# Kernel tuning notes

Measured on AMD Instinct MI355X. Metric: run time of the kernel, lower is better.

The kernel has to match this reference:

```python
import jax, jax.numpy as jnp
import numpy as np

T, OBS, H, NOBJ = 32768, 256, 512, 4


def _xavier(key, shape):
    fan_in, fan_out = shape[0], shape[1]
    lim = jnp.sqrt(6.0 / (fan_in + fan_out)).astype(jnp.float32)
    return jax.random.uniform(key, shape, jnp.float32, -lim, lim)


def setup_inputs() -> dict:
    key = jax.random.key(0)
    ks = jax.random.split(key, 16)
    # weights stored as [in, out] so y = x @ W (same math as nn.Linear with W.T)
    return {
        "x": jax.random.normal(ks[0], (T, OBS), jnp.float32),
        "W_in0": _xavier(ks[1], (OBS, H)),
        "W_B0": _xavier(ks[2], (OBS, H)),
        "W_C0": _xavier(ks[3], (OBS, H)),
        "W_d0": _xavier(ks[4], (OBS, H)),
        "A_log0": jax.random.normal(ks[5], (H,), jnp.float32),
        "W_in1": _xavier(ks[6], (H, H)),
        "W_B1": _xavier(ks[7], (H, H)),
        "W_C1": _xavier(ks[8], (H, H)),
        "W_d1": _xavier(ks[9], (H, H)),
        "A_log1": jax.random.normal(ks[10], (H,), jnp.float32),
        "W_out": _xavier(ks[11], (H, NOBJ)),
        "b_out": jnp.zeros((NOBJ,), jnp.float32),
        "W_skip": _xavier(ks[12], (OBS, NOBJ)),
    }


def _mamba_layer(x, W_in, W_B, W_C, W_d, A_log):
    # x: [T, D_in] -> [T, H]
    x_state = x @ W_in           # [T, H]
    B = x @ W_B                  # [T, H]
    C = x @ W_C                  # [T, H]
    delta = jax.nn.sigmoid(x @ W_d)  # [T, H]
    A = -jnp.exp(A_log)          # [H]
    A_bar = jnp.exp(delta * A)   # [T, H], in (0, 1)
    Bx = B * x_state             # [T, H]

    def step(h, inp):
        a_t, bx_t = inp
        h = a_t * h + bx_t
        return h, h

    h0 = jnp.zeros((x_state.shape[-1],), x_state.dtype)
    _, h_seq = jax.lax.scan(step, h0, (A_bar, Bx))  # [T, H]
    return C * h_seq


def reference(x, W_in0, W_B0, W_C0, W_d0, A_log0,
              W_in1, W_B1, W_C1, W_d1, A_log1,
              W_out, b_out, W_skip):
    skip = x
    y = _mamba_layer(x, W_in0, W_B0, W_C0, W_d0, A_log0)
    y = _mamba_layer(y, W_in1, W_B1, W_C1, W_d1, A_log1)
    out = y @ W_out + b_out + skip @ W_skip  # [T, NOBJ]
    return out
```

## Files before the change

### kernel.cpp

```cpp
#include <hip/hip_runtime.h>

typedef __attribute__((ext_vector_type(8))) short short8;
typedef __attribute__((ext_vector_type(4))) float floatx4;

#define T_SIZE 32768
#define OBS    256
#define H      512
#define NC     1024
#define CHUNK  32
#define NGRP   64
#define GCH    16

__device__ __forceinline__ unsigned short f2bf(float f){
    union { float f; unsigned u; } v; v.f = f;
    unsigned u = v.u;
    u += 0x7FFFu + ((u >> 16) & 1u);
    return (unsigned short)(u >> 16);
}
__device__ __forceinline__ float bf2f(unsigned short u){
    union { unsigned u; float f; } v; v.u = ((unsigned)u) << 16; return v.f;
}

#define GLOAD_LDS16(g, l) \
    __builtin_amdgcn_global_load_lds((const __attribute__((address_space(1))) unsigned*)(g), \
                                     (__attribute__((address_space(3))) unsigned*)(l), 16, 0, 0)

__global__ void prep_kernel(const float* __restrict__ x, unsigned short* __restrict__ xb,
                            const float* __restrict__ A0W0, const float* __restrict__ A0W1,
                            const float* __restrict__ A0W2, const float* __restrict__ A0W3,
                            unsigned short* __restrict__ Wt0,
                            const float* __restrict__ A1W0, const float* __restrict__ A1W1,
                            const float* __restrict__ A1W2, const float* __restrict__ A1W3,
                            unsigned short* __restrict__ Wt1){
    const int b = blockIdx.x;
    const int tid = threadIdx.x;
    if (b < 8192){
        int i = b * 256 + tid;
        float4 v = ((const float4*)x)[i];
        ushort4 o;
        o.x = f2bf(v.x); o.y = f2bf(v.y); o.z = f2bf(v.z); o.w = f2bf(v.w);
        ((ushort4*)xb)[i] = o;
    } else if (b < 10240){
        const int K = OBS, KH = OBS * H;
        int idx = (b - 8192) * 256 + tid;
        int s   = idx / KH;
        int rem = idx - s * KH;
        int h = rem >> 8;
        int k = rem & 255;
        const float* W = (s == 0) ? A0W0 : (s == 1) ? A0W1 : (s == 2) ? A0W2 : A0W3;
        int bb = h >> 4, hh = h & 15;
        Wt0[(size_t)((bb * 4 + s) * 16 + hh) * K + k] = f2bf(W[(size_t)k * H + h]);
    } else {
        const int K = H, KH = H * H;
        int idx = (b - 10240) * 256 + tid;
        int s   = idx / KH;
        int rem = idx - s * KH;
        int h = rem >> 9;
        int k = rem & 511;
        const float* W = (s == 0) ? A1W0 : (s == 1) ? A1W1 : (s == 2) ? A1W2 : A1W3;
        int bb = h >> 4, hh = h & 15;
        Wt1[(size_t)((bb * 4 + s) * 16 + hh) * K + k] = f2bf(W[(size_t)k * H + h]);
    }
}

template<int K>
__global__ __launch_bounds__(256, 3) void gemm_layer_kernel(
    const unsigned short* __restrict__ xb,
    const unsigned short* __restrict__ wt,
    const float* __restrict__ A_log,
    unsigned short* __restrict__ gT, unsigned short* __restrict__ bxT, unsigned short* __restrict__ CT,
    float* __restrict__ Pbuf, float* __restrict__ Hbuf,
    float* __restrict__ Pm, float* __restrict__ Hm)
{
    __shared__ unsigned short SM[3][8192];

    const int tid  = threadIdx.x;
    const int wave = tid >> 6;
    const int lane = tid & 63;
    const int ml   = lane & 15;
    const int quad = lane >> 4;
    const int wm   = wave & 1;
    const int wn   = wave >> 1;

    const int flat = blockIdx.y * 16 + blockIdx.x;
    const int xcd  = flat & 7;
    const int j    = flat >> 3;
    const int nb   = j & 15;
    const int mb   = (j >> 4) * 8 + xcd;
    const int m0   = mb * 128;

    const int srow = tid >> 2;
    const int sel  = (((tid & 3) ^ ((tid >> 3) & 3))) * 8;
    const int swz  = (ml >> 1) & 3;

    const unsigned short* pa0 = xb + (size_t)(m0 + srow) * K + sel;
    const unsigned short* pa1 = pa0 + (size_t)64 * K;
    const unsigned short* pb0 = wt + (size_t)(nb * 128 + srow) * K + sel;
    const unsigned short* pb1 = pb0 + (size_t)64 * K;

    const int ldsA0 = (wave * 64 + 0  ) * 8;
    const int ldsA1 = (wave * 64 + 256) * 8;

    const int rbaseA = (wm * 64 + ml) * 32 + (quad ^ swz) * 8;
    const int rbaseB = (wn * 64 + ml) * 32 + (quad ^ swz) * 8;

    floatx4 acc[4][4];
    #pragma unroll
    for (int i = 0; i < 4; i++)
        #pragma unroll
        for (int jj = 0; jj < 4; jj++)
            acc[i][jj] = (floatx4)(0.0f);

    constexpr int NK = K >> 5;

#define STAGE(kt_) { const int b_ = (kt_) % 3; const int ko_ = (kt_) * 32; \
        GLOAD_LDS16(pa0 + ko_, &SM[b_][ldsA0]); \
        GLOAD_LDS16(pa1 + ko_, &SM[b_][ldsA1]); \
        GLOAD_LDS16(pb0 + ko_, &SM[b_][4096 + ldsA0]); \
        GLOAD_LDS16(pb1 + ko_, &SM[b_][4096 + ldsA1]); }

    STAGE(0); STAGE(1);
    asm volatile("s_waitcnt vmcnt(4)" ::: "memory");
    __builtin_amdgcn_s_barrier();
    __builtin_amdgcn_sched_barrier(0);

    #pragma unroll
    for (int kk = 0; kk < NK; ++kk){
        const int cur = kk % 3;

        if (kk + 2 < NK) STAGE(kk + 2);

        short8 av[4], bv[4];
        #pragma unroll
        for (int i = 0; i < 4; i++)
            av[i] = *(const short8*)(&SM[cur][0] + rbaseA + i * 16 * 32);
        #pragma unroll
        for (int jj = 0; jj < 4; jj++)
            bv[jj] = *(const short8*)(&SM[cur][4096] + rbaseB + jj * 16 * 32);

        __builtin_amdgcn_s_setprio(1);
        #pragma unroll
        for (int i = 0; i < 4; i++)
            #pragma unroll
            for (int jj = 0; jj < 4; jj++)
                acc[i][jj] = __builtin_amdgcn_mfma_f32_16x16x32_bf16(av[i], bv[jj], acc[i][jj], 0, 0, 0);
        __builtin_amdgcn_s_setprio(0);

        if (kk + 1 < NK){
            if (kk + 2 < NK) { asm volatile("s_waitcnt vmcnt(4)" ::: "memory"); }
            else             { asm volatile("s_waitcnt vmcnt(0)" ::: "memory"); }
            __builtin_amdgcn_s_barrier();
            __builtin_amdgcn_sched_barrier(0);
        }
    }
    __syncthreads();

#undef STAGE

    unsigned short* SMe = &SM[0][0];
    float2* segbuf = (float2*)(SMe + 12288);
    const int col = wn * 16 + ml;
    const int h   = nb * 32 + col;
    const float Aneg = -expf(A_log[h]);

    #pragma unroll
    for (int i = 0; i < 4; i++){
        float p = 1.0f, hh = 0.0f;
        #pragma unroll
        for (int r = 0; r < 4; r++){
            int trow = wm * 64 + i * 16 + quad * 4 + r;
            float dv = acc[i][3][r];
            float delta = 1.0f / (1.0f + expf(-dv));
            unsigned short gb = f2bf(delta * Aneg);
            float a = __expf(bf2f(gb));
            unsigned short bb = f2bf(acc[i][1][r] * acc[i][0][r]);
            SMe[        trow * 32 + col] = gb;
            SMe[4096 +  trow * 32 + col] = bb;
            SMe[8192 +  trow * 32 + col] = f2bf(acc[i][2][r]);
            hh = fmaf(a, hh, bf2f(bb));
            p *= a;
        }
        const int ch = wm * 2 + (i >> 1);
        const int s  = (i & 1) * 4 + quad;
        segbuf[(ch * 8 + s) * 32 + col] = make_float2(p, hh);
    }
    __syncthreads();
    {
        const short8* s8 = (const short8*)SMe;
        #pragma unroll
        for (int arr = 0; arr < 3; arr++){
            unsigned short* bp = (arr == 0) ? gT : (arr == 1) ? bxT : CT;
            #pragma unroll
            for (int half = 0; half < 2; half++){
                int u = half * 256 + tid;
                int row = u >> 2, part = u & 3;
                *(short8*)(bp + (size_t)(m0 + row) * H + nb * 32 + part * 8) = s8[arr * 512 + u];
            }
        }
    }
    if (tid < 128){
        const int ccol = tid & 31, ch = tid >> 5;
        const int c = mb * 4 + ch;
        float P = 1.0f, Hc = 0.0f;
        #pragma unroll
        for (int s = 0; s < 4; s++){
            float2 ph = segbuf[(ch * 8 + s) * 32 + ccol];
            Hc = fmaf(ph.x, Hc, ph.y);
            P *= ph.x;
        }
        Pm[(size_t)c * H + nb * 32 + ccol] = P;
        Hm[(size_t)c * H + nb * 32 + ccol] = Hc;
        #pragma unroll
        for (int s = 4; s < 8; s++){
            float2 ph = segbuf[(ch * 8 + s) * 32 + ccol];
            Hc = fmaf(ph.x, Hc, ph.y);
            P *= ph.x;
        }
        Pbuf[(size_t)c * H + nb * 32 + ccol] = P;
        Hbuf[(size_t)c * H + nb * 32 + ccol] = Hc;
    }
}

__global__ void scan2a_kernel(const float* __restrict__ P, const float* __restrict__ Hc,
                              float* __restrict__ Pg, float* __restrict__ Hg){
    const int g  = blockIdx.x;
    const int j4 = threadIdx.x * 4;
    float4 pc = {1.f,1.f,1.f,1.f}, hc = {0.f,0.f,0.f,0.f};
    #pragma unroll
    for (int i = 0; i < GCH; i++){
        size_t o = (size_t)(g * GCH + i) * H + j4;
        float4 P4 = *(const float4*)(P + o);
        float4 H4 = *(const float4*)(Hc + o);
        hc.x = fmaf(P4.x, hc.x, H4.x); pc.x *= P4.x;
        hc.y = fmaf(P4.y, hc.y, H4.y); pc.y *= P4.y;
        hc.z = fmaf(P4.z, hc.z, H4.z); pc.z *= P4.z;
        hc.w = fmaf(P4.w, hc.w, H4.w); pc.w *= P4.w;
    }
    *(float4*)(Pg + (size_t)g * H + j4) = pc;
    *(float4*)(Hg + (size_t)g * H + j4) = hc;
}

__global__ __launch_bounds__(256) void scan3_kernel(
    const unsigned short* __restrict__ gT, const unsigned short* __restrict__ bxT,
    const unsigned short* __restrict__ CT,
    const float* __restrict__ P, const float* __restrict__ Hc,
    const float* __restrict__ Pm, const float* __restrict__ Hm,
    const float* __restrict__ Pg, const float* __restrict__ Hg,
    unsigned short* __restrict__ yb){
    const int c    = blockIdx.x;
    const int half = threadIdx.x >> 7;
    const int j4   = (threadIdx.x & 127) * 4;
    const int grp  = c >> 4;
    float4 h = {0.f, 0.f, 0.f, 0.f};
    for (int g = 0; g < grp; ++g){
        float4 P4 = *(const float4*)(Pg + (size_t)g * H + j4);
        float4 H4 = *(const float4*)(Hg + (size_t)g * H + j4);
        h.x = fmaf(P4.x, h.x, H4.x);
        h.y = fmaf(P4.y, h.y, H4.y);
        h.z = fmaf(P4.z, h.z, H4.z);
        h.w = fmaf(P4.w, h.w, H4.w);
    }
    for (int cc = grp << 4; cc < c; ++cc){
        float4 P4 = *(const float4*)(P + (size_t)cc * H + j4);
        float4 H4 = *(const float4*)(Hc + (size_t)cc * H + j4);
        h.x = fmaf(P4.x, h.x, H4.x);
        h.y = fmaf(P4.y, h.y, H4.y);
        h.z = fmaf(P4.z, h.z, H4.z);
        h.w = fmaf(P4.w, h.w, H4.w);
    }
    if (half){
        float4 P4 = *(const float4*)(Pm + (size_t)c * H + j4);
        float4 H4 = *(const float4*)(Hm + (size_t)c * H + j4);
        h.x = fmaf(P4.x, h.x, H4.x);
        h.y = fmaf(P4.y, h.y, H4.y);
        h.z = fmaf(P4.z, h.z, H4.z);
        h.w = fmaf(P4.w, h.w, H4.w);
    }
    size_t off = (size_t)(c * CHUNK + half * 16) * H + j4;
    #pragma unroll 8
    for (int i = 0; i < 16; i++){
        ushort4 gv = *(const ushort4*)(gT + off);
        ushort4 bv = *(const ushort4*)(bxT + off);
        ushort4 cv = *(const ushort4*)(CT + off);
        h.x = fmaf(__expf(bf2f(gv.x)), h.x, bf2f(bv.x));
        h.y = fmaf(__expf(bf2f(gv.y)), h.y, bf2f(bv.y));
        h.z = fmaf(__expf(bf2f(gv.z)), h.z, bf2f(bv.z));
        h.w = fmaf(__expf(bf2f(gv.w)), h.w, bf2f(bv.w));
        ushort4 o;
        o.x = f2bf(bf2f(cv.x) * h.x);
        o.y = f2bf(bf2f(cv.y) * h.y);
        o.z = f2bf(bf2f(cv.z) * h.z);
        o.w = f2bf(bf2f(cv.w) * h.w);
        *(ushort4*)(yb + off) = o;
        off += H;
    }
}

__global__ __launch_bounds__(256) void scan3f_kernel(
    const unsigned short* __restrict__ gT, const unsigned short* __restrict__ bxT,
    const unsigned short* __restrict__ CT,
    const float* __restrict__ P, const float* __restrict__ Hc,
    const float* __restrict__ Pm, const float* __restrict__ Hm,
    const float* __restrict__ Pg, const float* __restrict__ Hg,
    const unsigned short* __restrict__ xb,
    const float* __restrict__ Wout, const float* __restrict__ bout,
    const float* __restrict__ Wskip,
    float* __restrict__ out){
    __shared__ unsigned short ystage[32 * 512];
    const int tid  = threadIdx.x;
    const int c    = blockIdx.x;
    const int half = tid >> 7;
    const int j4   = (tid & 127) * 4;
    const int grp  = c >> 4;
    float4 h = {0.f, 0.f, 0.f, 0.f};
    for (int g = 0; g < grp; ++g){
        float4 P4 = *(const float4*)(Pg + (size_t)g * H + j4);
        float4 H4 = *(const float4*)(Hg + (size_t)g * H + j4);
        h.x = fmaf(P4.x, h.x, H4.x);
        h.y = fmaf(P4.y, h.y, H4.y);
        h.z = fmaf(P4.z, h.z, H4.z);
        h.w = fmaf(P4.w, h.w, H4.w);
    }
    for (int cc = grp << 4; cc < c; ++cc){
        float4 P4 = *(const float4*)(P + (size_t)cc * H + j4);
        float4 H4 = *(const float4*)(Hc + (size_t)cc * H + j4);
        h.x = fmaf(P4.x, h.x, H4.x);
        h.y = fmaf(P4.y, h.y, H4.y);
        h.z = fmaf(P4.z, h.z, H4.z);
        h.w = fmaf(P4.w, h.w, H4.w);
    }
    if (half){
        float4 P4 = *(const float4*)(Pm + (size_t)c * H + j4);
        float4 H4 = *(const float4*)(Hm + (size_t)c * H + j4);
        h.x = fmaf(P4.x, h.x, H4.x);
        h.y = fmaf(P4.y, h.y, H4.y);
        h.z = fmaf(P4.z, h.z, H4.z);
        h.w = fmaf(P4.w, h.w, H4.w);
    }
    size_t off = (size_t)(c * CHUNK + half * 16) * H + j4;
    #pragma unroll 8
    for (int i = 0; i < 16; i++){
        ushort4 gv = *(const ushort4*)(gT + off);
        ushort4 bv = *(const ushort4*)(bxT + off);
        ushort4 cv = *(const ushort4*)(CT + off);
        h.x = fmaf(__expf(bf2f(gv.x)), h.x, bf2f(bv.x));
        h.y = fmaf(__expf(bf2f(gv.y)), h.y, bf2f(bv.y));
        h.z = fmaf(__expf(bf2f(gv.z)), h.z, bf2f(bv.z));
        h.w = fmaf(__expf(bf2f(gv.w)), h.w, bf2f(bv.w));
        ushort4 o;
        o.x = f2bf(bf2f(cv.x) * h.x);
        o.y = f2bf(bf2f(cv.y) * h.y);
        o.z = f2bf(bf2f(cv.z) * h.z);
        o.w = f2bf(bf2f(cv.w) * h.w);
        *(ushort4*)(&ystage[(half * 16 + i) * 512 + j4]) = o;
        off += H;
    }
    __syncthreads();

    const int wave = tid >> 6;
    const int lane = tid & 63;
    const float4* W4 = (const float4*)Wout;
    const float4* S4 = (const float4*)Wskip;
    const float b0 = bout[0], b1 = bout[1], b2 = bout[2], b3 = bout[3];
    for (int rr = 0; rr < 8; ++rr){
        const int r = wave * 8 + rr;
        const int t = c * 32 + r;
        float s0 = 0.f, s1 = 0.f, s2 = 0.f, s3 = 0.f;
        #pragma unroll
        for (int k = lane; k < H; k += 64){
            float yv = bf2f(ystage[r * 512 + k]);
            float4 w = W4[k];
            s0 = fmaf(yv, w.x, s0); s1 = fmaf(yv, w.y, s1);
            s2 = fmaf(yv, w.z, s2); s3 = fmaf(yv, w.w, s3);
        }
        #pragma unroll
        for (int k = lane; k < OBS; k += 64){
            float xv = bf2f(xb[(size_t)t * OBS + k]);
            float4 w = S4[k];
            s0 = fmaf(xv, w.x, s0); s1 = fmaf(xv, w.y, s1);
            s2 = fmaf(xv, w.z, s2); s3 = fmaf(xv, w.w, s3);
        }
        #pragma unroll
        for (int o = 32; o > 0; o >>= 1){
            s0 += __shfl_down(s0, o);
            s1 += __shfl_down(s1, o);
            s2 += __shfl_down(s2, o);
            s3 += __shfl_down(s3, o);
        }
        if (lane == 0){
            out[(size_t)t * 4 + 0] = s0 + b0;
            out[(size_t)t * 4 + 1] = s1 + b1;
            out[(size_t)t * 4 + 2] = s2 + b2;
            out[(size_t)t * 4 + 3] = s3 + b3;
        }
    }
}

extern "C" void kernel_launch(void* const* d_in, const int* in_sizes, int n_in,
                              void* d_out, int out_size, void* d_ws, size_t ws_size,
                              hipStream_t stream)
{
    const float* x     = (const float*)d_in[0];
    const float* W_in0 = (const float*)d_in[1];
    const float* W_B0  = (const float*)d_in[2];
    const float* W_C0  = (const float*)d_in[3];
    const float* W_d0  = (const float*)d_in[4];
    const float* A0    = (const float*)d_in[5];
    const float* W_in1 = (const float*)d_in[6];
    const float* W_B1  = (const float*)d_in[7];
    const float* W_C1  = (const float*)d_in[8];
    const float* W_d1  = (const float*)d_in[9];
    const float* A1    = (const float*)d_in[10];
    const float* Wout  = (const float*)d_in[11];
    const float* bout  = (const float*)d_in[12];
    const float* Wskip = (const float*)d_in[13];
    float* out = (float*)d_out;

    char* ws = (char*)d_ws;
    size_t off = 0;
    auto alloc = [&](size_t bytes) -> void* {
        void* p = ws + off;
        off += (bytes + 255) & ~(size_t)255;
        return p;
    };
    unsigned short* xb  = (unsigned short*)alloc((size_t)T_SIZE * OBS * 2);
    unsigned short* yb  = (unsigned short*)alloc((size_t)T_SIZE * H * 2);
    unsigned short* Wt0 = (unsigned short*)alloc((size_t)4 * H * OBS * 2);
    unsigned short* Wt1 = (unsigned short*)alloc((size_t)4 * H * H * 2);
    unsigned short* gT  = (unsigned short*)alloc((size_t)T_SIZE * H * 2);
    unsigned short* bxT = (unsigned short*)alloc((size_t)T_SIZE * H * 2);
    unsigned short* CT  = (unsigned short*)alloc((size_t)T_SIZE * H * 2);
    float* Pbuf = (float*)alloc((size_t)NC * H * 4);
    float* Hbuf = (float*)alloc((size_t)NC * H * 4);
    float* Pm   = (float*)alloc((size_t)NC * H * 4);
    float* Hm   = (float*)alloc((size_t)NC * H * 4);
    float* Pg   = (float*)alloc((size_t)NGRP * H * 4);
    float* Hg   = (float*)alloc((size_t)NGRP * H * 4);
    (void)ws_size; (void)in_sizes; (void)n_in; (void)out_size;

    prep_kernel<<<14336, 256, 0, stream>>>(x, xb,
                                           W_in0, W_B0, W_C0, W_d0, Wt0,
                                           W_in1, W_B1, W_C1, W_d1, Wt1);

    dim3 ggrid(16, 256);

    gemm_layer_kernel<OBS><<<ggrid, 256, 0, stream>>>(xb, Wt0, A0, gT, bxT, CT, Pbuf, Hbuf, Pm, Hm);
    scan2a_kernel<<<NGRP, 128, 0, stream>>>(Pbuf, Hbuf, Pg, Hg);
    scan3_kernel<<<NC, 256, 0, stream>>>(gT, bxT, CT, Pbuf, Hbuf, Pm, Hm, Pg, Hg, yb);

    gemm_layer_kernel<H><<<ggrid, 256, 0, stream>>>(yb, Wt1, A1, gT, bxT, CT, Pbuf, Hbuf, Pm, Hm);
    scan2a_kernel<<<NGRP, 128, 0, stream>>>(Pbuf, Hbuf, Pg, Hg);
    scan3f_kernel<<<NC, 256, 0, stream>>>(gT, bxT, CT, Pbuf, Hbuf, Pm, Hm, Pg, Hg,
                                          xb, Wout, bout, Wskip, out);
}
```

Baseline: 313.3 us.

## Compute in-chunk local scan in GEMM epilogue and store affine correction terms

```diff
diff --git a/kernel.cpp b/kernel.cpp
--- a/kernel.cpp
+++ b/kernel.cpp
@@ -68,9 +68,8 @@
     const unsigned short* __restrict__ xb,
     const unsigned short* __restrict__ wt,
     const float* __restrict__ A_log,
-    unsigned short* __restrict__ gT, unsigned short* __restrict__ bxT, unsigned short* __restrict__ CT,
-    float* __restrict__ Pbuf, float* __restrict__ Hbuf,
-    float* __restrict__ Pm, float* __restrict__ Hm)
+    unsigned short* __restrict__ ylT, unsigned short* __restrict__ wT,
+    float* __restrict__ Pbuf, float* __restrict__ Hbuf)
 {
     __shared__ unsigned short SM[3][8192];
 
@@ -163,21 +162,18 @@
     const int h   = nb * 32 + col;
     const float Aneg = -expf(A_log[h]);
 
+    float va[4][4], vb[4][4], vc[4][4];
     #pragma unroll
     for (int i = 0; i < 4; i++){
         float p = 1.0f, hh = 0.0f;
         #pragma unroll
         for (int r = 0; r < 4; r++){
-            int trow = wm * 64 + i * 16 + quad * 4 + r;
             float dv = acc[i][3][r];
-            float delta = 1.0f / (1.0f + expf(-dv));
-            unsigned short gb = f2bf(delta * Aneg);
-            float a = __expf(bf2f(gb));
-            unsigned short bb = f2bf(acc[i][1][r] * acc[i][0][r]);
-            SMe[        trow * 32 + col] = gb;
-            SMe[4096 +  trow * 32 + col] = bb;
-            SMe[8192 +  trow * 32 + col] = f2bf(acc[i][2][r]);
-            hh = fmaf(a, hh, bf2f(bb));
+            float delta = 1.0f / (1.0f + __expf(-dv));
+            float a  = __expf(delta * Aneg);
+            float bx = acc[i][1][r] * acc[i][0][r];
+            va[i][r] = a; vb[i][r] = bx; vc[i][r] = acc[i][2][r];
+            hh = fmaf(a, hh, bx);
             p *= a;
         }
         const int ch = wm * 2 + (i >> 1);
@@ -185,11 +181,46 @@
         segbuf[(ch * 8 + s) * 32 + col] = make_float2(p, hh);
     }
     __syncthreads();
+
+    #pragma unroll
+    for (int i = 0; i < 4; i++){
+        const int ch = wm * 2 + (i >> 1);
+        const int s  = (i & 1) * 4 + quad;
+        float Pexc = 1.0f, Hexc = 0.0f;
+        for (int sp = 0; sp < s; sp++){
+            float2 ph = segbuf[(ch * 8 + sp) * 32 + col];
+            Hexc = fmaf(ph.x, Hexc, ph.y);
+            Pexc *= ph.x;
+        }
+        float hcur = Hexc, pf = Pexc;
+        #pragma unroll
+        for (int r = 0; r < 4; r++){
+            hcur = fmaf(va[i][r], hcur, vb[i][r]);
+            pf  *= va[i][r];
+            int trow = wm * 64 + i * 16 + quad * 4 + r;
+            SMe[        trow * 32 + col] = f2bf(vc[i][r] * hcur);
+            SMe[4096 +  trow * 32 + col] = f2bf(vc[i][r] * pf);
+        }
+    }
+    if (tid < 128){
+        const int ccol = tid & 31, ch = tid >> 5;
+        float P = 1.0f, Hc = 0.0f;
+        #pragma unroll
+        for (int s = 0; s < 8; s++){
+            float2 ph = segbuf[(ch * 8 + s) * 32 + ccol];
+            Hc = fmaf(ph.x, Hc, ph.y);
+            P *= ph.x;
+        }
+        const int c = mb * 4 + ch;
+        Pbuf[(size_t)c * H + nb * 32 + ccol] = P;
+        Hbuf[(size_t)c * H + nb * 32 + ccol] = Hc;
+    }
+    __syncthreads();
     {
         const short8* s8 = (const short8*)SMe;
         #pragma unroll
-        for (int arr = 0; arr < 3; arr++){
-            unsigned short* bp = (arr == 0) ? gT : (arr == 1) ? bxT : CT;
+        for (int arr = 0; arr < 2; arr++){
+            unsigned short* bp = (arr == 0) ? ylT : wT;
             #pragma unroll
             for (int half = 0; half < 2; half++){
                 int u = half * 256 + tid;
@@ -197,27 +228,6 @@
                 *(short8*)(bp + (size_t)(m0 + row) * H + nb * 32 + part * 8) = s8[arr * 512 + u];
             }
         }
-    }
-    if (tid < 128){
-        const int ccol = tid & 31, ch = tid >> 5;
-        const int c = mb * 4 + ch;
-        float P = 1.0f, Hc = 0.0f;
-        #pragma unroll
-        for (int s = 0; s < 4; s++){
-            float2 ph = segbuf[(ch * 8 + s) * 32 + ccol];
-            Hc = fmaf(ph.x, Hc, ph.y);
-            P *= ph.x;
-        }
-        Pm[(size_t)c * H + nb * 32 + ccol] = P;
-        Hm[(size_t)c * H + nb * 32 + ccol] = Hc;
-        #pragma unroll
-        for (int s = 4; s < 8; s++){
-            float2 ph = segbuf[(ch * 8 + s) * 32 + ccol];
-            Hc = fmaf(ph.x, Hc, ph.y);
-            P *= ph.x;
-        }
-        Pbuf[(size_t)c * H + nb * 32 + ccol] = P;
-        Hbuf[(size_t)c * H + nb * 32 + ccol] = Hc;
     }
 }
 
@@ -241,10 +251,8 @@
 }
 
 __global__ __launch_bounds__(256) void scan3_kernel(
-    const unsigned short* __restrict__ gT, const unsigned short* __restrict__ bxT,
-    const unsigned short* __restrict__ CT,
+    const unsigned short* __restrict__ ylT, const unsigned short* __restrict__ wT,
     const float* __restrict__ P, const float* __restrict__ Hc,
-    const float* __restrict__ Pm, const float* __restrict__ Hm,
     const float* __restrict__ Pg, const float* __restrict__ Hg,
     unsigned short* __restrict__ yb){
     const int c    = blockIdx.x;
@@ -268,39 +276,24 @@
         h.z = fmaf(P4.z, h.z, H4.z);
         h.w = fmaf(P4.w, h.w, H4.w);
     }
-    if (half){
-        float4 P4 = *(const float4*)(Pm + (size_t)c * H + j4);
-        float4 H4 = *(const float4*)(Hm + (size_t)c * H + j4);
-        h.x = fmaf(P4.x, h.x, H4.x);
-        h.y = fmaf(P4.y, h.y, H4.y);
-        h.z = fmaf(P4.z, h.z, H4.z);
-        h.w = fmaf(P4.w, h.w, H4.w);
-    }
     size_t off = (size_t)(c * CHUNK + half * 16) * H + j4;
     #pragma unroll 8
     for (int i = 0; i < 16; i++){
-        ushort4 gv = *(const ushort4*)(gT + off);
-        ushort4 bv = *(const ushort4*)(bxT + off);
-        ushort4 cv = *(const ushort4*)(CT + off);
-        h.x = fmaf(__expf(bf2f(gv.x)), h.x, bf2f(bv.x));
-        h.y = fmaf(__expf(bf2f(gv.y)), h.y, bf2f(bv.y));
-        h.z = fmaf(__expf(bf2f(gv.z)), h.z, bf2f(bv.z));
-        h.w = fmaf(__expf(bf2f(gv.w)), h.w, bf2f(bv.w));
+        ushort4 yl = *(const ushort4*)(ylT + off);
+        ushort4 w4 = *(const ushort4*)(wT + off);
         ushort4 o;
-        o.x = f2bf(bf2f(cv.x) * h.x);
-        o.y = f2bf(bf2f(cv.y) * h.y);
-        o.z = f2bf(bf2f(cv.z) * h.z);
-        o.w = f2bf(bf2f(cv.w) * h.w);
+        o.x = f2bf(fmaf(bf2f(w4.x), h.x, bf2f(yl.x)));
+        o.y = f2bf(fmaf(bf2f(w4.y), h.y, bf2f(yl.y)));
+        o.z = f2bf(fmaf(bf2f(w4.z), h.z, bf2f(yl.z)));
+        o.w = f2bf(fmaf(bf2f(w4.w), h.w, bf2f(yl.w)));
         *(ushort4*)(yb + off) = o;
         off += H;
     }
 }
 
 __global__ __launch_bounds__(256) void scan3f_kernel(
-    const unsigned short* __restrict__ gT, const unsigned short* __restrict__ bxT,
-    const unsigned short* __restrict__ CT,
+    const unsigned short* __restrict__ ylT, const unsigned short* __restrict__ wT,
     const float* __restrict__ P, const float* __restrict__ Hc,
-    const float* __restrict__ Pm, const float* __restrict__ Hm,
     const float* __restrict__ Pg, const float* __restrict__ Hg,
     const unsigned short* __restrict__ xb,
     const float* __restrict__ Wout, const float* __restrict__ bout,
@@ -329,29 +322,16 @@
         h.z = fmaf(P4.z, h.z, H4.z);
         h.w = fmaf(P4.w, h.w, H4.w);
     }
-    if (half){
-        float4 P4 = *(const float4*)(Pm + (size_t)c * H + j4);
-        float4 H4 = *(const float4*)(Hm + (size_t)c * H + j4);
-        h.x = fmaf(P4.x, h.x, H4.x);
-        h.y = fmaf(P4.y, h.y, H4.y);
-        h.z = fmaf(P4.z, h.z, H4.z);
-        h.w = fmaf(P4.w, h.w, H4.w);
-    }
     size_t off = (size_t)(c * CHUNK + half * 16) * H + j4;
     #pragma unroll 8
     for (int i = 0; i < 16; i++){
-        ushort4 gv = *(const ushort4*)(gT + off);
-        ushort4 bv = *(const ushort4*)(bxT + off);
-        ushort4 cv = *(const ushort4*)(CT + off);
-        h.x = fmaf(__expf(bf2f(gv.x)), h.x, bf2f(bv.x));
-        h.y = fmaf(__expf(bf2f(gv.y)), h.y, bf2f(bv.y));
-        h.z = fmaf(__expf(bf2f(gv.z)), h.z, bf2f(bv.z));
-        h.w = fmaf(__expf(bf2f(gv.w)), h.w, bf2f(bv.w));
+        ushort4 yl = *(const ushort4*)(ylT + off);
+        ushort4 w4 = *(const ushort4*)(wT + off);
         ushort4 o;
-        o.x = f2bf(bf2f(cv.x) * h.x);
-        o.y = f2bf(bf2f(cv.y) * h.y);
-        o.z = f2bf(bf2f(cv.z) * h.z);
-        o.w = f2bf(bf2f(cv.w) * h.w);
+        o.x = f2bf(fmaf(bf2f(w4.x), h.x, bf2f(yl.x)));
+        o.y = f2bf(fmaf(bf2f(w4.y), h.y, bf2f(yl.y)));
+        o.z = f2bf(fmaf(bf2f(w4.z), h.z, bf2f(yl.z)));
+        o.w = f2bf(fmaf(bf2f(w4.w), h.w, bf2f(yl.w)));
         *(ushort4*)(&ystage[(half * 16 + i) * 512 + j4]) = o;
         off += H;
     }
@@ -427,13 +407,10 @@
     unsigned short* yb  = (unsigned short*)alloc((size_t)T_SIZE * H * 2);
     unsigned short* Wt0 = (unsigned short*)alloc((size_t)4 * H * OBS * 2);
     unsigned short* Wt1 = (unsigned short*)alloc((size_t)4 * H * H * 2);
-    unsigned short* gT  = (unsigned short*)alloc((size_t)T_SIZE * H * 2);
-    unsigned short* bxT = (unsigned short*)alloc((size_t)T_SIZE * H * 2);
-    unsigned short* CT  = (unsigned short*)alloc((size_t)T_SIZE * H * 2);
+    unsigned short* ylT = (unsigned short*)alloc((size_t)T_SIZE * H * 2);
+    unsigned short* wT  = (unsigned short*)alloc((size_t)T_SIZE * H * 2);
     float* Pbuf = (float*)alloc((size_t)NC * H * 4);
     float* Hbuf = (float*)alloc((size_t)NC * H * 4);
-    float* Pm   = (float*)alloc((size_t)NC * H * 4);
-    float* Hm   = (float*)alloc((size_t)NC * H * 4);
     float* Pg   = (float*)alloc((size_t)NGRP * H * 4);
     float* Hg   = (float*)alloc((size_t)NGRP * H * 4);
     (void)ws_size; (void)in_sizes; (void)n_in; (void)out_size;
@@ -444,12 +421,12 @@
 
     dim3 ggrid(16, 256);
 
-    gemm_layer_kernel<OBS><<<ggrid, 256, 0, stream>>>(xb, Wt0, A0, gT, bxT, CT, Pbuf, Hbuf, Pm, Hm);
+    gemm_layer_kernel<OBS><<<ggrid, 256, 0, stream>>>(xb, Wt0, A0, ylT, wT, Pbuf, Hbuf);
     scan2a_kernel<<<NGRP, 128, 0, stream>>>(Pbuf, Hbuf, Pg, Hg);
-    scan3_kernel<<<NC, 256, 0, stream>>>(gT, bxT, CT, Pbuf, Hbuf, Pm, Hm, Pg, Hg, yb);
-
-    gemm_layer_kernel<H><<<ggrid, 256, 0, stream>>>(yb, Wt1, A1, gT, bxT, CT, Pbuf, Hbuf, Pm, Hm);
+    scan3_kernel<<<NC, 256, 0, stream>>>(ylT, wT, Pbuf, Hbuf, Pg, Hg, yb);
+
+    gemm_layer_kernel<H><<<ggrid, 256, 0, stream>>>(yb, Wt1, A1, ylT, wT, Pbuf, Hbuf);
     scan2a_kernel<<<NGRP, 128, 0, stream>>>(Pbuf, Hbuf, Pg, Hg);
-    scan3f_kernel<<<NC, 256, 0, stream>>>(gT, bxT, CT, Pbuf, Hbuf, Pm, Hm, Pg, Hg,
+    scan3f_kernel<<<NC, 256, 0, stream>>>(ylT, wT, Pbuf, Hbuf, Pg, Hg,
                                           xb, Wout, bout, Wskip, out);
 }
```

Measured after the change: 305.3 us. 2.5% less time.
